# Kernel optimization log

Hardware: AMD Instinct MI355X
Metric: run time of the kernel (lower is better)

The kernel has to match this reference:

```python
import jax, jax.numpy as jnp
jax.config.update("jax_enable_x64", True)
import numpy as np

N_E = 8192      # codebook size
E_DIM = 512     # code dim
BETA = 0.25
SK_EPS = 0.003
SK_ITERS = 5
N_TOK = 8192


def sinkhorn(d, eps, iters):
    # d: [B, K] centered distances in float64 (matches torch .double())
    Q = jnp.exp(-d / eps).T            # [K, B]
    K, B = Q.shape
    Q = Q / Q.sum()

    def body(Q, _):
        Q = Q / Q.sum(axis=1, keepdims=True) / K   # normalize rows (codes)
        Q = Q / Q.sum(axis=0, keepdims=True) / B   # normalize cols (tokens)
        return Q, None

    Q, _ = jax.lax.scan(body, Q, None, length=iters)
    Q = Q * B
    return Q.T                          # [B, K]


def setup_inputs() -> dict:
    key = jax.random.key(0)
    k1, k2 = jax.random.split(key)
    x = jax.random.normal(k1, (N_TOK, E_DIM), dtype=jnp.float32)
    # nn.Embedding weight init: uniform(-1/n_e, 1/n_e)
    emb = jax.random.uniform(k2, (N_E, E_DIM), dtype=jnp.float32,
                             minval=-1.0 / N_E, maxval=1.0 / N_E)
    return {"x": x, "emb": emb}


def reference(x, emb):
    latent = x.reshape(-1, E_DIM)                                  # [B, D]
    # pairwise squared L2: ||z||^2 + ||e||^2 - 2 z e^T  -> [B, K]
    d = (jnp.sum(latent ** 2, axis=1, keepdims=True)
         + jnp.sum(emb ** 2, axis=1)[None, :]
         - 2.0 * latent @ emb.T)
    # center_distance_for_constraint
    mx = d.max()
    mn = d.min()
    middle = (mx + mn) / 2
    amplitude = mx - middle + 1e-5
    dc = ((d - middle) / amplitude).astype(jnp.float64)
    Q = sinkhorn(dc, SK_EPS, SK_ITERS)
    indices = jnp.argmax(Q, axis=-1)                               # [B]
    x_q = emb[indices].reshape(x.shape)
    codebook_loss = jnp.mean((x_q - jax.lax.stop_gradient(x)) ** 2)
    commitment_loss = jnp.mean((jax.lax.stop_gradient(x_q) - x) ** 2)
    loss = codebook_loss + BETA * commitment_loss
    # straight-through estimator
    x_q_st = x + jax.lax.stop_gradient(x_q - x)
    return x_q_st, loss, indices.reshape(x.shape[:-1])
```

## Files before the change

kernel.cpp:

```cpp
#include <hip/hip_runtime.h>
#include <cfloat>
#include <cstdint>
#include <cstddef>

#define NTOK 8192
#define NE   8192
#define DIM  512
#define OUT0 4194304

__device__ __forceinline__ double fexp_d(double x){
  const double L2E = 1.4426950408889634074;
  const double LN2 = 0.69314718055994530942;
  double kd = rint(x * L2E);
  double r  = fma(-kd, LN2, x);
  double p = 2.4801587301587301566e-05;
  p = fma(p, r, 1.9841269841269841253e-04);
  p = fma(p, r, 1.3888888888888889419e-03);
  p = fma(p, r, 8.3333333333333332177e-03);
  p = fma(p, r, 4.1666666666666664354e-02);
  p = fma(p, r, 1.6666666666666665741e-01);
  p = fma(p, r, 5.0e-01);
  p = fma(p, r, 1.0);
  p = fma(p, r, 1.0);
  long long eb = ((long long)(1023 + (int)kd)) << 52;
  return p * __longlong_as_double(eb);
}

__device__ __forceinline__ unsigned int f2ord(float f){
  unsigned int u = __float_as_uint(f);
  return (u & 0x80000000u) ? ~u : (u | 0x80000000u);
}
__device__ __forceinline__ float ord2f(unsigned int v){
  unsigned int u = (v & 0x80000000u) ? (v ^ 0x80000000u) : ~v;
  return __uint_as_float(u);
}

__device__ float pw128_sq(const float* __restrict__ p){
  float r[8];
#pragma unroll
  for (int j = 0; j < 8; ++j) r[j] = __fmul_rn(p[j], p[j]);
#pragma unroll
  for (int i = 8; i < 128; i += 8)
#pragma unroll
    for (int j = 0; j < 8; ++j) r[j] = __fadd_rn(r[j], __fmul_rn(p[i+j], p[i+j]));
  float s01 = __fadd_rn(r[0], r[1]), s23 = __fadd_rn(r[2], r[3]);
  float s45 = __fadd_rn(r[4], r[5]), s67 = __fadd_rn(r[6], r[7]);
  return __fadd_rn(__fadd_rn(s01, s23), __fadd_rn(s45, s67));
}
__device__ float pw512_sq(const float* __restrict__ p){
  float s0 = __fadd_rn(pw128_sq(p),       pw128_sq(p + 128));
  float s1 = __fadd_rn(pw128_sq(p + 256), pw128_sq(p + 384));
  return __fadd_rn(s0, s1);
}

__global__ void normsK(const float* __restrict__ src, float* __restrict__ dst, int n){
  int i = blockIdx.x * blockDim.x + threadIdx.x;
  if (i < n) dst[i] = pw512_sq(src + (size_t)i * DIM);
}

__global__ void initK(unsigned int* sc32){
  if (threadIdx.x == 0){ sc32[0] = 0u; sc32[1] = 0xFFFFFFFFu; }
}

__global__ void finalizeK(const unsigned int* sc32, float* scf){
  if (threadIdx.x == 0){
    float mx = ord2f(sc32[0]);
    float mn = ord2f(sc32[1]);
    float middle = __fmul_rn(__fadd_rn(mx, mn), 0.5f);
    float amp    = __fadd_rn(__fsub_rn(mx, middle), 1e-5f);
    scf[0] = middle; scf[1] = amp;
  }
}

__global__ void diagK(float* __restrict__ out, int n, float tag){
  int i = blockIdx.x * blockDim.x + threadIdx.x;
  int stride = gridDim.x * blockDim.x;
  for (; i < n; i += stride) out[i] = (i == OUT0) ? tag : 0.f;
}

#define GBM 128
#define GBN 128
#define GBK 32
#define GLDT 132
__global__ __launch_bounds__(256, 4) void gemm128(const float* __restrict__ X, const float* __restrict__ E,
    const float* __restrict__ avec, const float* __restrict__ hvec,
    float* __restrict__ dmat, unsigned int* __restrict__ sc32){
  __shared__ float As[GBK][GLDT];
  __shared__ float Bs[GBK][GLDT];
  __shared__ float red[256];
  int tid = threadIdx.x;
  int tx = tid & 15, ty = tid >> 4;
  int bm = blockIdx.y * GBM, bn = blockIdx.x * GBN;

  float acc[8][8];
#pragma unroll
  for (int i = 0; i < 8; ++i)
#pragma unroll
    for (int j = 0; j < 8; ++j) acc[i][j] = 0.f;

  for (int kt = 0; kt < DIM; kt += GBK){
#pragma unroll
    for (int s = 0; s < 4; ++s){
      int flat = tid + s * 256;
      int m  = flat >> 3;
      int k4 = (flat & 7) * 4;
      float4 va = *(const float4*)(X + (size_t)(bm + m) * DIM + kt + k4);
      As[k4+0][m] = va.x; As[k4+1][m] = va.y; As[k4+2][m] = va.z; As[k4+3][m] = va.w;
      float4 vb = *(const float4*)(E + (size_t)(bn + m) * DIM + kt + k4);
      Bs[k4+0][m] = vb.x; Bs[k4+1][m] = vb.y; Bs[k4+2][m] = vb.z; Bs[k4+3][m] = vb.w;
    }
    __syncthreads();
#pragma unroll
    for (int kk = 0; kk < GBK; ++kk){
      float a[8], b[8];
      *(float4*)&a[0] = *(const float4*)&As[kk][ty * 8];
      *(float4*)&a[4] = *(const float4*)&As[kk][ty * 8 + 4];
      *(float4*)&b[0] = *(const float4*)&Bs[kk][tx * 8];
      *(float4*)&b[4] = *(const float4*)&Bs[kk][tx * 8 + 4];
#pragma unroll
      for (int i = 0; i < 8; ++i)
#pragma unroll
        for (int j = 0; j < 8; ++j)
          acc[i][j] = fmaf(a[i], b[j], acc[i][j]);
    }
    __syncthreads();
  }

  float lmax = -FLT_MAX, lmin = FLT_MAX;
#pragma unroll
  for (int i = 0; i < 8; ++i){
    int gr = bm + ty * 8 + i;
    float a = avec[gr];
    float dv[8];
#pragma unroll
    for (int j = 0; j < 8; ++j){
      int gc = bn + tx * 8 + j;
      float t = __fadd_rn(a, hvec[gc]);
      float d = __fsub_rn(t, 2.0f * acc[i][j]);
      dv[j] = d;
      lmax = fmaxf(lmax, d); lmin = fminf(lmin, d);
    }
    *(float4*)(dmat + (size_t)gr * NE + bn + tx * 8)     = *(float4*)&dv[0];
    *(float4*)(dmat + (size_t)gr * NE + bn + tx * 8 + 4) = *(float4*)&dv[4];
  }
  red[tid] = lmax; __syncthreads();
  for (int s = 128; s > 0; s >>= 1){ if (tid < s) red[tid] = fmaxf(red[tid], red[tid+s]); __syncthreads(); }
  float bmax = red[0];
  __syncthreads();
  red[tid] = lmin; __syncthreads();
  for (int s = 128; s > 0; s >>= 1){ if (tid < s) red[tid] = fminf(red[tid], red[tid+s]); __syncthreads(); }
  if (tid == 0){
    atomicMax(&sc32[0], f2ord(bmax));
    atomicMin(&sc32[1], f2ord(red[0]));
  }
}

__global__ __launch_bounds__(256) void rowPassK(const float* __restrict__ dmat, const double* __restrict__ wvec,
    const float* __restrict__ scf, double* __restrict__ partials){
  int tid = threadIdx.x;
  int k0 = blockIdx.x * 512 + tid * 2;
  int b0 = blockIdx.y * 256;
  float middle = scf[0], amp = scf[1];
  const double NIE = -(1.0 / 0.003);
  const float* p = dmat + (size_t)b0 * NE + k0;
  double a0 = 0.0, a1 = 0.0;
  if (wvec){
    for (int bb = 0; bb < 256; bb += 4){
      float2 v0 = *(const float2*)(p + (size_t)(bb+0) * NE);
      float2 v1 = *(const float2*)(p + (size_t)(bb+1) * NE);
      float2 v2 = *(const float2*)(p + (size_t)(bb+2) * NE);
      float2 v3 = *(const float2*)(p + (size_t)(bb+3) * NE);
      double w0 = wvec[b0+bb+0], w1 = wvec[b0+bb+1], w2 = wvec[b0+bb+2], w3 = wvec[b0+bb+3];
      a0 = fma(fexp_d((double)__fdiv_rn(__fsub_rn(v0.x, middle), amp) * NIE), w0, a0);
      a1 = fma(fexp_d((double)__fdiv_rn(__fsub_rn(v0.y, middle), amp) * NIE), w0, a1);
      a0 = fma(fexp_d((double)__fdiv_rn(__fsub_rn(v1.x, middle), amp) * NIE), w1, a0);
      a1 = fma(fexp_d((double)__fdiv_rn(__fsub_rn(v1.y, middle), amp) * NIE), w1, a1);
      a0 = fma(fexp_d((double)__fdiv_rn(__fsub_rn(v2.x, middle), amp) * NIE), w2, a0);
      a1 = fma(fexp_d((double)__fdiv_rn(__fsub_rn(v2.y, middle), amp) * NIE), w2, a1);
      a0 = fma(fexp_d((double)__fdiv_rn(__fsub_rn(v3.x, middle), amp) * NIE), w3, a0);
      a1 = fma(fexp_d((double)__fdiv_rn(__fsub_rn(v3.y, middle), amp) * NIE), w3, a1);
    }
  } else {
    for (int bb = 0; bb < 256; bb += 4){
      float2 v0 = *(const float2*)(p + (size_t)(bb+0) * NE);
      float2 v1 = *(const float2*)(p + (size_t)(bb+1) * NE);
      float2 v2 = *(const float2*)(p + (size_t)(bb+2) * NE);
      float2 v3 = *(const float2*)(p + (size_t)(bb+3) * NE);
      a0 += fexp_d((double)__fdiv_rn(__fsub_rn(v0.x, middle), amp) * NIE);
      a1 += fexp_d((double)__fdiv_rn(__fsub_rn(v0.y, middle), amp) * NIE);
      a0 += fexp_d((double)__fdiv_rn(__fsub_rn(v1.x, middle), amp) * NIE);
      a1 += fexp_d((double)__fdiv_rn(__fsub_rn(v1.y, middle), amp) * NIE);
      a0 += fexp_d((double)__fdiv_rn(__fsub_rn(v2.x, middle), amp) * NIE);
      a1 += fexp_d((double)__fdiv_rn(__fsub_rn(v2.y, middle), amp) * NIE);
      a0 += fexp_d((double)__fdiv_rn(__fsub_rn(v3.x, middle), amp) * NIE);
      a1 += fexp_d((double)__fdiv_rn(__fsub_rn(v3.y, middle), amp) * NIE);
    }
  }
  partials[(size_t)blockIdx.y * NE + k0]     = a0;
  partials[(size_t)blockIdx.y * NE + k0 + 1] = a1;
}

__global__ void reduceAK(const double* __restrict__ partials, double* __restrict__ ak){
  int k = blockIdx.x * 256 + threadIdx.x;
  double s = 0.0;
  for (int c = 0; c < 32; ++c) s += partials[(size_t)c * NE + k];
  ak[k] = 1.0 / (8192.0 * s);
}

__global__ __launch_bounds__(256) void colPassK(const float* __restrict__ dmat, const double* __restrict__ ak,
    const float* __restrict__ scf, double* __restrict__ bvec){
  __shared__ double sd[256];
  int b = blockIdx.x, tid = threadIdx.x;
  float middle = scf[0], amp = scf[1];
  const double NIE = -(1.0 / 0.003);
  const float* row = dmat + (size_t)b * NE;
  double acc = 0.0;
  for (int kb = 0; kb < 32; kb += 4){
    int k0 = tid + (kb+0) * 256, k1 = tid + (kb+1) * 256, k2 = tid + (kb+2) * 256, k3 = tid + (kb+3) * 256;
    float r0 = row[k0], r1 = row[k1], r2 = row[k2], r3 = row[k3];
    double q0 = ak[k0], q1 = ak[k1], q2 = ak[k2], q3 = ak[k3];
    acc = fma(fexp_d((double)__fdiv_rn(__fsub_rn(r0, middle), amp) * NIE), q0, acc);
    acc = fma(fexp_d((double)__fdiv_rn(__fsub_rn(r1, middle), amp) * NIE), q1, acc);
    acc = fma(fexp_d((double)__fdiv_rn(__fsub_rn(r2, middle), amp) * NIE), q2, acc);
    acc = fma(fexp_d((double)__fdiv_rn(__fsub_rn(r3, middle), amp) * NIE), q3, acc);
  }
  sd[tid] = acc; __syncthreads();
  for (int s = 128; s > 0; s >>= 1){ if (tid < s) sd[tid] += sd[tid+s]; __syncthreads(); }
  if (tid == 0) bvec[b] = 1.0 / (8192.0 * sd[0]);
}

__global__ void lnaK(const double* __restrict__ ak, double* __restrict__ lna){
  int k = blockIdx.x * 256 + threadIdx.x;
  lna[k] = log(ak[k]);
}

__global__ __launch_bounds__(256) void argmaxK(const float* __restrict__ dmat, const double* __restrict__ lna,
    const float* __restrict__ scf, float* __restrict__ idxF){
  __shared__ double sv[256];
  __shared__ int    si[256];
  int b = blockIdx.x, tid = threadIdx.x;
  float middle = scf[0], amp = scf[1];
  const double NIE = -(1.0 / 0.003);
  const float* row = dmat + (size_t)b * NE;
  double best = -1.0e300; int bk = NE;
#pragma unroll 2
  for (int c = 0; c < 8; ++c){
    int k = c * 1024 + tid * 4;
    float4 v = *(const float4*)(row + k);
    double l0 = lna[k], l1 = lna[k+1], l2 = lna[k+2], l3 = lna[k+3];
    double t0 = fma((double)__fdiv_rn(__fsub_rn(v.x, middle), amp), NIE, l0);
    double t1 = fma((double)__fdiv_rn(__fsub_rn(v.y, middle), amp), NIE, l1);
    double t2 = fma((double)__fdiv_rn(__fsub_rn(v.z, middle), amp), NIE, l2);
    double t3 = fma((double)__fdiv_rn(__fsub_rn(v.w, middle), amp), NIE, l3);
    if (t0 > best){ best = t0; bk = k; }
    if (t1 > best){ best = t1; bk = k+1; }
    if (t2 > best){ best = t2; bk = k+2; }
    if (t3 > best){ best = t3; bk = k+3; }
  }
  sv[tid] = best; si[tid] = bk; __syncthreads();
  for (int s = 128; s > 0; s >>= 1){
    if (tid < s){
      double o = sv[tid+s]; int ok = si[tid+s];
      if (o > sv[tid] || (o == sv[tid] && ok < si[tid])){ sv[tid] = o; si[tid] = ok; }
    }
    __syncthreads();
  }
  if (tid == 0) idxF[b] = (float)si[0];
}

__global__ __launch_bounds__(256) void lossK(const float* __restrict__ X, const float* __restrict__ E,
    const float* __restrict__ idxF, double* __restrict__ lparts){
  __shared__ double sd[256];
  int b = blockIdx.x, tid = threadIdx.x;
  int id = (int)idxF[b];
  const float* xr = X + (size_t)b * DIM;
  const float* er = E + (size_t)id * DIM;
  double ls = 0.0;
#pragma unroll
  for (int c = 0; c < 2; ++c){
    int dpos = tid + c * 256;
    float diff = __fsub_rn(er[dpos], xr[dpos]);
    ls = fma((double)diff, (double)diff, ls);
  }
  sd[tid] = ls; __syncthreads();
  for (int s = 128; s > 0; s >>= 1){ if (tid < s) sd[tid] += sd[tid+s]; __syncthreads(); }
  if (tid == 0) lparts[b] = sd[0];
}

__global__ __launch_bounds__(256) void lossFinK(const double* __restrict__ lparts, float* __restrict__ lossOut){
  __shared__ double sd[256];
  int tid = threadIdx.x;
  double s = 0.0;
  for (int b = tid; b < NTOK; b += 256) s += lparts[b];
  sd[tid] = s; __syncthreads();
  for (int st = 128; st > 0; st >>= 1){ if (tid < st) sd[tid] += sd[tid+st]; __syncthreads(); }
  if (tid == 0){
    double v = sd[0] / (double)((size_t)NTOK * DIM);
    float vf = (float)v;
    lossOut[0] = __fadd_rn(vf, __fmul_rn(0.25f, vf));
  }
}

__global__ __launch_bounds__(256) void out0K(const float* __restrict__ X, const float* __restrict__ E,
    const float* __restrict__ idxF, float* __restrict__ out0){
  int b = blockIdx.x, tid = threadIdx.x;
  int id = (int)idxF[b];
  const float* xr = X + (size_t)b * DIM;
  const float* er = E + (size_t)id * DIM;
#pragma unroll
  for (int c = 0; c < 2; ++c){
    int dpos = tid + c * 256;
    float xv = xr[dpos];
    float diff = __fsub_rn(er[dpos], xv);
    out0[(size_t)b * DIM + dpos] = __fadd_rn(xv, diff);
  }
}

extern "C" void kernel_launch(void* const* d_in, const int* in_sizes, int n_in,
                              void* d_out, int out_size, void* d_ws, size_t ws_size,
                              hipStream_t stream){
  (void)in_sizes; (void)n_in;
  const float* X = (const float*)d_in[0];
  const float* E = (const float*)d_in[1];
  float* out = (float*)d_out;

  if (ws_size < 268435456ull || d_ws == nullptr){
    diagK<<<2048, 256, 0, stream>>>(out, out_size, (float)(ws_size >> 20));
    return;
  }
  float* dmat = (float*)d_ws;

  float*  avec   = out;
  float*  hvec   = out + 8192;
  double* parts  = (double*)(out + 16384);
  double* ak     = (double*)(out + 540672);
  double* bvec   = (double*)(out + 557056);
  double* lna    = (double*)(out + 573440);
  unsigned int* sc32 = (unsigned int*)(out + 589824);
  float*  scf    = out + 589826;
  double* lparts = parts;

  float* out0    = out;
  float* lossOut = out + OUT0;
  float* idxF    = out + OUT0 + 1;

  initK<<<1, 64, 0, stream>>>(sc32);
  normsK<<<32, 256, 0, stream>>>(X, avec, NTOK);
  normsK<<<32, 256, 0, stream>>>(E, hvec, NE);

  dim3 gg(NE / GBN, NTOK / GBM);
  gemm128<<<gg, 256, 0, stream>>>(X, E, avec, hvec, dmat, sc32);
  finalizeK<<<1, 64, 0, stream>>>(sc32, scf);

  dim3 rp(16, 32);
  rowPassK<<<rp, 256, 0, stream>>>(dmat, nullptr, scf, parts);
  reduceAK<<<32, 256, 0, stream>>>(parts, ak);
  for (int it = 0; it < 4; ++it){
    colPassK<<<NTOK, 256, 0, stream>>>(dmat, ak, scf, bvec);
    rowPassK<<<rp, 256, 0, stream>>>(dmat, bvec, scf, parts);
    reduceAK<<<32, 256, 0, stream>>>(parts, ak);
  }

  lnaK<<<32, 256, 0, stream>>>(ak, lna);
  argmaxK<<<NTOK, 256, 0, stream>>>(dmat, lna, scf, idxF);
  lossK<<<NTOK, 256, 0, stream>>>(X, E, idxF, lparts);
  lossFinK<<<1, 256, 0, stream>>>(lparts, lossOut);
  out0K<<<NTOK, 256, 0, stream>>>(X, E, idxF, out0);
}
```

Measured before the change: 1.538 ms.

## Remap GEMM thread tiles, widen row pass, fuse norms and argmax with loss

Splits each thread's 8x8 GEMM micro-tile into two 4x4 halves strided by 64 so LDS reads and global stores are less conflicted and better coalesced. The Sinkhorn row pass now processes four codes per thread with float4 loads on half as many blocks. The two norm launches are merged into one, and the argmax and loss kernels are fused to avoid a launch and a reread of indices. Fewer blocks in the row pass may reduce occupancy and latency hiding.

```diff
diff --git a/kernel.cpp b/kernel.cpp
--- a/kernel.cpp
+++ b/kernel.cpp
@@ -53,9 +53,12 @@
   return __fadd_rn(s0, s1);
 }
 
-__global__ void normsK(const float* __restrict__ src, float* __restrict__ dst, int n){
-  int i = blockIdx.x * blockDim.x + threadIdx.x;
-  if (i < n) dst[i] = pw512_sq(src + (size_t)i * DIM);
+__global__ __launch_bounds__(256) void normsK(const float* __restrict__ X, const float* __restrict__ E,
+    float* __restrict__ avec, float* __restrict__ hvec){
+  int blk = blockIdx.x;
+  int i = (blk & 31) * 256 + threadIdx.x;
+  if (blk < 32) avec[i] = pw512_sq(X + (size_t)i * DIM);
+  else          hvec[i] = pw512_sq(E + (size_t)i * DIM);
 }
 
 __global__ void initK(unsigned int* sc32){
@@ -92,11 +95,15 @@
   int tx = tid & 15, ty = tid >> 4;
   int bm = blockIdx.y * GBM, bn = blockIdx.x * GBN;
 
-  float acc[8][8];
-#pragma unroll
-  for (int i = 0; i < 8; ++i)
-#pragma unroll
-    for (int j = 0; j < 8; ++j) acc[i][j] = 0.f;
+  float acc[2][4][2][4];
+#pragma unroll
+  for (int ih = 0; ih < 2; ++ih)
+#pragma unroll
+    for (int i = 0; i < 4; ++i)
+#pragma unroll
+      for (int jh = 0; jh < 2; ++jh)
+#pragma unroll
+        for (int j = 0; j < 4; ++j) acc[ih][i][jh][j] = 0.f;
 
   for (int kt = 0; kt < DIM; kt += GBK){
 #pragma unroll
@@ -112,36 +119,45 @@
     __syncthreads();
 #pragma unroll
     for (int kk = 0; kk < GBK; ++kk){
-      float a[8], b[8];
-      *(float4*)&a[0] = *(const float4*)&As[kk][ty * 8];
-      *(float4*)&a[4] = *(const float4*)&As[kk][ty * 8 + 4];
-      *(float4*)&b[0] = *(const float4*)&Bs[kk][tx * 8];
-      *(float4*)&b[4] = *(const float4*)&Bs[kk][tx * 8 + 4];
-#pragma unroll
-      for (int i = 0; i < 8; ++i)
-#pragma unroll
-        for (int j = 0; j < 8; ++j)
-          acc[i][j] = fmaf(a[i], b[j], acc[i][j]);
+      float a[2][4], b[2][4];
+      *(float4*)a[0] = *(const float4*)&As[kk][ty * 4];
+      *(float4*)a[1] = *(const float4*)&As[kk][64 + ty * 4];
+      *(float4*)b[0] = *(const float4*)&Bs[kk][tx * 4];
+      *(float4*)b[1] = *(const float4*)&Bs[kk][64 + tx * 4];
+#pragma unroll
+      for (int ih = 0; ih < 2; ++ih)
+#pragma unroll
+        for (int i = 0; i < 4; ++i)
+#pragma unroll
+          for (int jh = 0; jh < 2; ++jh)
+#pragma unroll
+            for (int j = 0; j < 4; ++j)
+              acc[ih][i][jh][j] = fmaf(a[ih][i], b[jh][j], acc[ih][i][jh][j]);
     }
     __syncthreads();
   }
 
   float lmax = -FLT_MAX, lmin = FLT_MAX;
 #pragma unroll
-  for (int i = 0; i < 8; ++i){
-    int gr = bm + ty * 8 + i;
-    float a = avec[gr];
-    float dv[8];
-#pragma unroll
-    for (int j = 0; j < 8; ++j){
-      int gc = bn + tx * 8 + j;
-      float t = __fadd_rn(a, hvec[gc]);
-      float d = __fsub_rn(t, 2.0f * acc[i][j]);
-      dv[j] = d;
-      lmax = fmaxf(lmax, d); lmin = fminf(lmin, d);
-    }
-    *(float4*)(dmat + (size_t)gr * NE + bn + tx * 8)     = *(float4*)&dv[0];
-    *(float4*)(dmat + (size_t)gr * NE + bn + tx * 8 + 4) = *(float4*)&dv[4];
+  for (int ih = 0; ih < 2; ++ih){
+#pragma unroll
+    for (int i = 0; i < 4; ++i){
+      int gr = bm + ih * 64 + ty * 4 + i;
+      float a = avec[gr];
+#pragma unroll
+      for (int jh = 0; jh < 2; ++jh){
+        float dv[4];
+#pragma unroll
+        for (int j = 0; j < 4; ++j){
+          int gc = bn + jh * 64 + tx * 4 + j;
+          float t = __fadd_rn(a, hvec[gc]);
+          float d = __fsub_rn(t, 2.0f * acc[ih][i][jh][j]);
+          dv[j] = d;
+          lmax = fmaxf(lmax, d); lmin = fminf(lmin, d);
+        }
+        *(float4*)(dmat + (size_t)gr * NE + bn + jh * 64 + tx * 4) = *(float4*)&dv[0];
+      }
+    }
   }
   red[tid] = lmax; __syncthreads();
   for (int s = 128; s > 0; s >>= 1){ if (tid < s) red[tid] = fmaxf(red[tid], red[tid+s]); __syncthreads(); }
@@ -155,49 +171,37 @@
   }
 }
 
+#define EXPD(x) fexp_d((double)__fdiv_rn(__fsub_rn((x), middle), amp) * NIE)
+
 __global__ __launch_bounds__(256) void rowPassK(const float* __restrict__ dmat, const double* __restrict__ wvec,
     const float* __restrict__ scf, double* __restrict__ partials){
   int tid = threadIdx.x;
-  int k0 = blockIdx.x * 512 + tid * 2;
+  int k0 = blockIdx.x * 1024 + tid * 4;
   int b0 = blockIdx.y * 256;
   float middle = scf[0], amp = scf[1];
   const double NIE = -(1.0 / 0.003);
   const float* p = dmat + (size_t)b0 * NE + k0;
-  double a0 = 0.0, a1 = 0.0;
+  double a0 = 0.0, a1 = 0.0, a2 = 0.0, a3 = 0.0;
   if (wvec){
-    for (int bb = 0; bb < 256; bb += 4){
-      float2 v0 = *(const float2*)(p + (size_t)(bb+0) * NE);
-      float2 v1 = *(const float2*)(p + (size_t)(bb+1) * NE);
-      float2 v2 = *(const float2*)(p + (size_t)(bb+2) * NE);
-      float2 v3 = *(const float2*)(p + (size_t)(bb+3) * NE);
-      double w0 = wvec[b0+bb+0], w1 = wvec[b0+bb+1], w2 = wvec[b0+bb+2], w3 = wvec[b0+bb+3];
-      a0 = fma(fexp_d((double)__fdiv_rn(__fsub_rn(v0.x, middle), amp) * NIE), w0, a0);
-      a1 = fma(fexp_d((double)__fdiv_rn(__fsub_rn(v0.y, middle), amp) * NIE), w0, a1);
-      a0 = fma(fexp_d((double)__fdiv_rn(__fsub_rn(v1.x, middle), amp) * NIE), w1, a0);
-      a1 = fma(fexp_d((double)__fdiv_rn(__fsub_rn(v1.y, middle), amp) * NIE), w1, a1);
-      a0 = fma(fexp_d((double)__fdiv_rn(__fsub_rn(v2.x, middle), amp) * NIE), w2, a0);
-      a1 = fma(fexp_d((double)__fdiv_rn(__fsub_rn(v2.y, middle), amp) * NIE), w2, a1);
-      a0 = fma(fexp_d((double)__fdiv_rn(__fsub_rn(v3.x, middle), amp) * NIE), w3, a0);
-      a1 = fma(fexp_d((double)__fdiv_rn(__fsub_rn(v3.y, middle), amp) * NIE), w3, a1);
+    for (int bb = 0; bb < 256; bb += 2){
+      float4 v0 = *(const float4*)(p + (size_t)(bb+0) * NE);
+      float4 v1 = *(const float4*)(p + (size_t)(bb+1) * NE);
+      double w0 = wvec[b0+bb+0], w1 = wvec[b0+bb+1];
+      a0 = fma(EXPD(v0.x), w0, a0); a1 = fma(EXPD(v0.y), w0, a1);
+      a2 = fma(EXPD(v0.z), w0, a2); a3 = fma(EXPD(v0.w), w0, a3);
+      a0 = fma(EXPD(v1.x), w1, a0); a1 = fma(EXPD(v1.y), w1, a1);
+      a2 = fma(EXPD(v1.z), w1, a2); a3 = fma(EXPD(v1.w), w1, a3);
     }
   } else {
-    for (int bb = 0; bb < 256; bb += 4){
-      float2 v0 = *(const float2*)(p + (size_t)(bb+0) * NE);
-      float2 v1 = *(const float2*)(p + (size_t)(bb+1) * NE);
-      float2 v2 = *(const float2*)(p + (size_t)(bb+2) * NE);
-      float2 v3 = *(const float2*)(p + (size_t)(bb+3) * NE);
-      a0 += fexp_d((double)__fdiv_rn(__fsub_rn(v0.x, middle), amp) * NIE);
-      a1 += fexp_d((double)__fdiv_rn(__fsub_rn(v0.y, middle), amp) * NIE);
-      a0 += fexp_d((double)__fdiv_rn(__fsub_rn(v1.x, middle), amp) * NIE);
-      a1 += fexp_d((double)__fdiv_rn(__fsub_rn(v1.y, middle), amp) * NIE);
-      a0 += fexp_d((double)__fdiv_rn(__fsub_rn(v2.x, middle), amp) * NIE);
-      a1 += fexp_d((double)__fdiv_rn(__fsub_rn(v2.y, middle), amp) * NIE);
-      a0 += fexp_d((double)__fdiv_rn(__fsub_rn(v3.x, middle), amp) * NIE);
-      a1 += fexp_d((double)__fdiv_rn(__fsub_rn(v3.y, middle), amp) * NIE);
-    }
-  }
-  partials[(size_t)blockIdx.y * NE + k0]     = a0;
-  partials[(size_t)blockIdx.y * NE + k0 + 1] = a1;
+    for (int bb = 0; bb < 256; bb += 2){
+      float4 v0 = *(const float4*)(p + (size_t)(bb+0) * NE);
+      float4 v1 = *(const float4*)(p + (size_t)(bb+1) * NE);
+      a0 += EXPD(v0.x); a1 += EXPD(v0.y); a2 += EXPD(v0.z); a3 += EXPD(v0.w);
+      a0 += EXPD(v1.x); a1 += EXPD(v1.y); a2 += EXPD(v1.z); a3 += EXPD(v1.w);
+    }
+  }
+  double* q = partials + (size_t)blockIdx.y * NE + k0;
+  q[0] = a0; q[1] = a1; q[2] = a2; q[3] = a3;
 }
 
 __global__ void reduceAK(const double* __restrict__ partials, double* __restrict__ ak){
@@ -219,10 +223,10 @@
     int k0 = tid + (kb+0) * 256, k1 = tid + (kb+1) * 256, k2 = tid + (kb+2) * 256, k3 = tid + (kb+3) * 256;
     float r0 = row[k0], r1 = row[k1], r2 = row[k2], r3 = row[k3];
     double q0 = ak[k0], q1 = ak[k1], q2 = ak[k2], q3 = ak[k3];
-    acc = fma(fexp_d((double)__fdiv_rn(__fsub_rn(r0, middle), amp) * NIE), q0, acc);
-    acc = fma(fexp_d((double)__fdiv_rn(__fsub_rn(r1, middle), amp) * NIE), q1, acc);
-    acc = fma(fexp_d((double)__fdiv_rn(__fsub_rn(r2, middle), amp) * NIE), q2, acc);
-    acc = fma(fexp_d((double)__fdiv_rn(__fsub_rn(r3, middle), amp) * NIE), q3, acc);
+    acc = fma(EXPD(r0), q0, acc);
+    acc = fma(EXPD(r1), q1, acc);
+    acc = fma(EXPD(r2), q2, acc);
+    acc = fma(EXPD(r3), q3, acc);
   }
   sd[tid] = acc; __syncthreads();
   for (int s = 128; s > 0; s >>= 1){ if (tid < s) sd[tid] += sd[tid+s]; __syncthreads(); }
@@ -234,10 +238,12 @@
   lna[k] = log(ak[k]);
 }
 
-__global__ __launch_bounds__(256) void argmaxK(const float* __restrict__ dmat, const double* __restrict__ lna,
-    const float* __restrict__ scf, float* __restrict__ idxF){
+__global__ __launch_bounds__(256) void argmaxLossK(const float* __restrict__ dmat, const double* __restrict__ lna,
+    const float* __restrict__ scf, const float* __restrict__ X, const float* __restrict__ E,
+    float* __restrict__ idxF, double* __restrict__ lparts){
   __shared__ double sv[256];
   __shared__ int    si[256];
+  __shared__ int    sidx;
   int b = blockIdx.x, tid = threadIdx.x;
   float middle = scf[0], amp = scf[1];
   const double NIE = -(1.0 / 0.003);
@@ -265,14 +271,10 @@
     }
     __syncthreads();
   }
-  if (tid == 0) idxF[b] = (float)si[0];
-}
-
-__global__ __launch_bounds__(256) void lossK(const float* __restrict__ X, const float* __restrict__ E,
-    const float* __restrict__ idxF, double* __restrict__ lparts){
-  __shared__ double sd[256];
-  int b = blockIdx.x, tid = threadIdx.x;
-  int id = (int)idxF[b];
+  if (tid == 0){ idxF[b] = (float)si[0]; sidx = si[0]; }
+  __syncthreads();
+
+  int id = sidx;
   const float* xr = X + (size_t)b * DIM;
   const float* er = E + (size_t)id * DIM;
   double ls = 0.0;
@@ -282,9 +284,9 @@
     float diff = __fsub_rn(er[dpos], xr[dpos]);
     ls = fma((double)diff, (double)diff, ls);
   }
-  sd[tid] = ls; __syncthreads();
-  for (int s = 128; s > 0; s >>= 1){ if (tid < s) sd[tid] += sd[tid+s]; __syncthreads(); }
-  if (tid == 0) lparts[b] = sd[0];
+  sv[tid] = ls; __syncthreads();
+  for (int s = 128; s > 0; s >>= 1){ if (tid < s) sv[tid] += sv[tid+s]; __syncthreads(); }
+  if (tid == 0) lparts[b] = sv[0];
 }
 
 __global__ __launch_bounds__(256) void lossFinK(const double* __restrict__ lparts, float* __restrict__ lossOut){
@@ -345,14 +347,13 @@
   float* idxF    = out + OUT0 + 1;
 
   initK<<<1, 64, 0, stream>>>(sc32);
-  normsK<<<32, 256, 0, stream>>>(X, avec, NTOK);
-  normsK<<<32, 256, 0, stream>>>(E, hvec, NE);
+  normsK<<<64, 256, 0, stream>>>(X, E, avec, hvec);
 
   dim3 gg(NE / GBN, NTOK / GBM);
   gemm128<<<gg, 256, 0, stream>>>(X, E, avec, hvec, dmat, sc32);
   finalizeK<<<1, 64, 0, stream>>>(sc32, scf);
 
-  dim3 rp(16, 32);
+  dim3 rp(8, 32);
   rowPassK<<<rp, 256, 0, stream>>>(dmat, nullptr, scf, parts);
   reduceAK<<<32, 256, 0, stream>>>(parts, ak);
   for (int it = 0; it < 4; ++it){
@@ -362,8 +363,7 @@
   }
 
   lnaK<<<32, 256, 0, stream>>>(ak, lna);
-  argmaxK<<<NTOK, 256, 0, stream>>>(dmat, lna, scf, idxF);
-  lossK<<<NTOK, 256, 0, stream>>>(X, E, idxF, lparts);
+  argmaxLossK<<<NTOK, 256, 0, stream>>>(dmat, lna, scf, X, E, idxF, lparts);
   lossFinK<<<1, 256, 0, stream>>>(lparts, lossOut);
   out0K<<<NTOK, 256, 0, stream>>>(X, E, idxF, out0);
 }
```

Measured after the change: 1.638 ms. 1.07x slower.
